# Optimization experiments

Measured on AMD Instinct MI355X. Metric: run time of the kernel, lower is better.

The kernel has to match this reference:

```python
import jax, jax.numpy as jnp
import numpy as np

TEMPERATURE = 0.1
NORMALIZE = True
EPS = 1e-8  # matches torch F.normalize eps-free clamp behavior closely enough for randn inputs

B, D = 4096, 512


def setup_inputs() -> dict:
    key = jax.random.key(0)
    k1, k2 = jax.random.split(key)
    z_i = jax.random.normal(k1, (B, D), dtype=jnp.float32)
    z_j = jax.random.normal(k2, (B, D), dtype=jnp.float32)
    return {"z_i": z_i, "z_j": z_j}


def _l2_normalize(x):
    # torch.F.normalize: x / max(||x||, eps)
    n = jnp.linalg.norm(x, axis=1, keepdims=True)
    return x / jnp.maximum(n, 1e-12)


def reference(z_i, z_j):
    b = z_i.shape[0]
    if NORMALIZE:
        z_i = _l2_normalize(z_i)
        z_j = _l2_normalize(z_j)
    z = jnp.concatenate([z_i, z_j], axis=0)               # (2B, D)
    logits = (z @ z.T) / TEMPERATURE                      # (2B, 2B)
    n = 2 * b
    diag = jnp.eye(n, dtype=bool)
    logits = jnp.where(diag, -jnp.inf, logits)
    row = jnp.arange(n)
    pos_col = (row + b) % n
    pos_logits = logits[row, pos_col]                     # (2B,)
    lse = jax.scipy.special.logsumexp(logits, axis=1)     # stable logsumexp per row
    loss = -(pos_logits - lse).mean()
    return loss
```

## Files before the change

### kernel.cpp

```cpp
#include <hip/hip_runtime.h>
#include <stdint.h>

#define D_DIM 512
#define B_ROWS 4096
#define N_ROWS 8192
#define SCALE_L2E 14.426950408889634f

#define NHP 8
#define BM 128
#define NT (N_ROWS / BM)
#define NBLK 2080

typedef __attribute__((ext_vector_type(4))) float f32x4;
typedef __attribute__((ext_vector_type(2))) long f8x16;

__global__ __launch_bounds__(256) void k_normalize(const float* __restrict__ zi,
                                                   const float* __restrict__ zj,
                                                   unsigned char* __restrict__ Zn,
                                                   float* __restrict__ pos) {
    const int t = threadIdx.x;
    const int lane = t & 63;
    const int i = blockIdx.x * 4 + (t >> 6);
    const float* pa = zi + (size_t)i * D_DIM + lane * 8;
    const float* pb = zj + (size_t)i * D_DIM + lane * 8;
    const float4 a0 = *(const float4*)pa;
    const float4 a1 = *(const float4*)(pa + 4);
    const float4 b0 = *(const float4*)pb;
    const float4 b1 = *(const float4*)(pb + 4);
    float ssi = a0.x*a0.x + a0.y*a0.y + a0.z*a0.z + a0.w*a0.w
              + a1.x*a1.x + a1.y*a1.y + a1.z*a1.z + a1.w*a1.w;
    float ssj = b0.x*b0.x + b0.y*b0.y + b0.z*b0.z + b0.w*b0.w
              + b1.x*b1.x + b1.y*b1.y + b1.z*b1.z + b1.w*b1.w;
    float dt  = a0.x*b0.x + a0.y*b0.y + a0.z*b0.z + a0.w*b0.w
              + a1.x*b1.x + a1.y*b1.y + a1.z*b1.z + a1.w*b1.w;
    #pragma unroll
    for (int off = 1; off < 64; off <<= 1) {
        ssi += __shfl_xor(ssi, off);
        ssj += __shfl_xor(ssj, off);
        dt  += __shfl_xor(dt,  off);
    }
    const float si = 1.0f / fmaxf(sqrtf(ssi), 1e-12f);
    const float sj = 1.0f / fmaxf(sqrtf(ssj), 1e-12f);
    uint2 pi8, pj8;
    {
        int w0 = 0, w1 = 0;
        w0 = __builtin_amdgcn_cvt_pk_fp8_f32(a0.x * si, a0.y * si, w0, false);
        w0 = __builtin_amdgcn_cvt_pk_fp8_f32(a0.z * si, a0.w * si, w0, true);
        w1 = __builtin_amdgcn_cvt_pk_fp8_f32(a1.x * si, a1.y * si, w1, false);
        w1 = __builtin_amdgcn_cvt_pk_fp8_f32(a1.z * si, a1.w * si, w1, true);
        pi8.x = (unsigned)w0; pi8.y = (unsigned)w1;
        w0 = 0; w1 = 0;
        w0 = __builtin_amdgcn_cvt_pk_fp8_f32(b0.x * sj, b0.y * sj, w0, false);
        w0 = __builtin_amdgcn_cvt_pk_fp8_f32(b0.z * sj, b0.w * sj, w0, true);
        w1 = __builtin_amdgcn_cvt_pk_fp8_f32(b1.x * sj, b1.y * sj, w1, false);
        w1 = __builtin_amdgcn_cvt_pk_fp8_f32(b1.z * sj, b1.w * sj, w1, true);
        pj8.x = (unsigned)w0; pj8.y = (unsigned)w1;
    }
    const size_t PLANE = (size_t)N_ROWS * 64;
    const int o = lane & 7;
    const size_t off0 = (size_t)(lane >> 3) * PLANE + (o & 3) * 16 + (o >> 2) * 8;
    *(uint2*)(Zn + off0 + (size_t)i * 64) = pi8;
    *(uint2*)(Zn + off0 + (size_t)(B_ROWS + i) * 64) = pj8;
    if (lane == 0) pos[i] = 20.0f * dt * si * sj;
}

__global__ __launch_bounds__(256, 4) void k_gemm_lse(const unsigned char* __restrict__ Zn,
                                                     float* __restrict__ rowsum_g) {
    const int t    = threadIdx.x;
    const int lane = t & 63;
    const int w    = t >> 6;
    const int wm   = w >> 1, wn = w & 1;
    const int l15  = lane & 15, lhi = lane >> 4;

    int g = (blockIdx.x & 7) * (NBLK / 8) + (blockIdx.x >> 3);
    int SI = 0, SJ = 0;
    {
        bool found = false;
        for (SI = 0; SI < 8 && !found; ++SI) {
            for (SJ = SI; SJ < 8; ++SJ) {
                const int sz = (SI == SJ) ? 36 : 64;
                if (g < sz) { found = true; break; }
                g -= sz;
            }
        }
        --SI;
    }
    int di, dj;
    if (SI == SJ) {
        di = 0;
        while (g >= 8 - di) { g -= 8 - di; ++di; }
        dj = di + g;
    } else {
        di = g >> 3; dj = g & 7;
    }
    const int I = SI * 8 + di, J = SJ * 8 + dj;
    const bool dg = (I == J);
    const int rowB = I * BM + wm * 64;
    const int colB = J * BM + wn * 64;

    const char* Zb = (const char*)Zn;
    const size_t PLANE = (size_t)N_ROWS * 64;

    const char* pA = Zb + ((size_t)(rowB + l15)) * 64 + lhi * 16;
    const char* pB = Zb + ((size_t)(colB + l15)) * 64 + lhi * 16;

    f32x4 acc[4][4];
    #pragma unroll
    for (int a = 0; a < 4; ++a)
        #pragma unroll
        for (int b = 0; b < 4; ++b)
            #pragma unroll
            for (int q = 0; q < 4; ++q) acc[a][b][q] = 0.0f;

    for (int hp = 0; hp < NHP; ++hp) {
        f8x16 af[4], bg[4];
        const char* _a = pA + (size_t)hp * PLANE;
        const char* _b = pB + (size_t)hp * PLANE;
        #pragma unroll
        for (int mi = 0; mi < 4; ++mi) af[mi] = *(const f8x16*)(_a + mi * 1024);
        #pragma unroll
        for (int ni = 0; ni < 4; ++ni) bg[ni] = *(const f8x16*)(_b + ni * 1024);
        __builtin_amdgcn_s_setprio(1);
        #pragma unroll
        for (int mi = 0; mi < 4; ++mi)
            #pragma unroll
            for (int ni = 0; ni < 4; ++ni)
                acc[mi][ni] = __builtin_amdgcn_mfma_f32_16x16x32_fp8_fp8(
                    af[mi][0], bg[ni][0], acc[mi][ni], 0, 0, 0);
        #pragma unroll
        for (int mi = 0; mi < 4; ++mi)
            #pragma unroll
            for (int ni = 0; ni < 4; ++ni)
                acc[mi][ni] = __builtin_amdgcn_mfma_f32_16x16x32_fp8_fp8(
                    af[mi][1], bg[ni][1], acc[mi][ni], 0, 0, 0);
        __builtin_amdgcn_s_setprio(0);
    }

    float colsum[4] = {0.0f, 0.0f, 0.0f, 0.0f};
    #pragma unroll
    for (int mi = 0; mi < 4; ++mi) {
        const int growb = rowB + mi * 16 + lhi * 4;
        float rs[4] = {0.0f, 0.0f, 0.0f, 0.0f};
        if (dg && wm == wn) {
            #pragma unroll
            for (int ni = 0; ni < 4; ++ni) {
                const int gcol = colB + ni * 16 + l15;
                #pragma unroll
                for (int r = 0; r < 4; ++r) {
                    float arg = acc[mi][ni][r] * SCALE_L2E;
                    if (growb + r == gcol) arg = -1e30f;
                    rs[r] += exp2f(arg);
                }
            }
        } else {
            #pragma unroll
            for (int ni = 0; ni < 4; ++ni)
                #pragma unroll
                for (int r = 0; r < 4; ++r) {
                    const float e = exp2f(acc[mi][ni][r] * SCALE_L2E);
                    rs[r] += e;
                    colsum[ni] += e;
                }
        }
        #pragma unroll
        for (int r = 0; r < 4; ++r) {
            float v = rs[r];
            v += __shfl_xor(v, 1);
            v += __shfl_xor(v, 2);
            v += __shfl_xor(v, 4);
            v += __shfl_xor(v, 8);
            if (l15 == 0) atomicAdd(&rowsum_g[growb + r], v);
        }
    }
    if (!dg ? true : (wm < wn)) {
        if (!(dg && wm == wn)) {
            #pragma unroll
            for (int ni = 0; ni < 4; ++ni) {
                float c = colsum[ni];
                c += __shfl_xor(c, 16);
                c += __shfl_xor(c, 32);
                if (lhi == 0)
                    atomicAdd(&rowsum_g[colB + ni * 16 + l15], c);
            }
        }
    }
}

__global__ __launch_bounds__(1024) void k_finalize(const float* __restrict__ rowsum_g,
                                                   const float* __restrict__ pos,
                                                   float* __restrict__ out) {
    const int t = threadIdx.x;
    float l = 0.0f, p = 0.0f;
    #pragma unroll
    for (int q = 0; q < N_ROWS / 1024; ++q) l += logf(rowsum_g[t + q * 1024]);
    #pragma unroll
    for (int q = 0; q < B_ROWS / 1024; ++q) p += pos[t + q * 1024];
    #pragma unroll
    for (int off = 1; off < 64; off <<= 1) {
        l += __shfl_xor(l, off);
        p += __shfl_xor(p, off);
    }
    __shared__ float red[2][16];
    if ((t & 63) == 0) { red[0][t >> 6] = l; red[1][t >> 6] = p; }
    __syncthreads();
    if (t == 0) {
        float L = 0.0f, P = 0.0f;
        #pragma unroll
        for (int q = 0; q < 16; ++q) { L += red[0][q]; P += red[1][q]; }
        out[0] = (L - P) * (1.0f / (float)N_ROWS);
    }
}

extern "C" void kernel_launch(void* const* d_in, const int* in_sizes, int n_in,
                              void* d_out, int out_size, void* d_ws, size_t ws_size,
                              hipStream_t stream) {
    (void)in_sizes; (void)n_in; (void)out_size; (void)ws_size;
    const float* zi = (const float*)d_in[0];
    const float* zj = (const float*)d_in[1];

    const size_t ZN_BYTES = (size_t)N_ROWS * D_DIM;
    unsigned char* Zn     = (unsigned char*)d_ws;
    float* rowsum_g       = (float*)((char*)d_ws + ZN_BYTES);
    float* pos            = (float*)((char*)d_ws + ZN_BYTES + N_ROWS * 4);

    hipMemsetAsync(rowsum_g, 0, N_ROWS * 4, stream);

    k_normalize<<<B_ROWS / 4, 256, 0, stream>>>(zi, zj, Zn, pos);
    k_gemm_lse<<<NBLK, 256, 0, stream>>>(Zn, rowsum_g);
    k_finalize<<<1, 1024, 0, stream>>>(rowsum_g, pos, (float*)d_out);
}
```

Before: 61.96 us.

## Stage FP8 panels through LDS with async global_load_lds multi-stage pipeline

The GEMM kernel now copies 128-row A and B panels into an 8-slot LDS ring with global_load_lds, keeping five stages in flight, instead of each wave loading its fragments straight from global memory. The fp8 layout changes to 16 planes of 32 bytes per row to match the K=32 MFMA steps. The rowsum memset is folded into the normalize kernel. The aim is to share panel loads across the block's waves and hide global latency, at the cost of 64KB of LDS per block, which cuts occupancy to 2 blocks, and a barrier on every step.

```diff
diff --git a/kernel.cpp b/kernel.cpp
--- a/kernel.cpp
+++ b/kernel.cpp
@@ -6,19 +6,26 @@
 #define N_ROWS 8192
 #define SCALE_L2E 14.426950408889634f
 
-#define NHP 8
-#define BM 128
-#define NT (N_ROWS / BM)
+#define NST 16
 #define NBLK 2080
 
 typedef __attribute__((ext_vector_type(4))) float f32x4;
-typedef __attribute__((ext_vector_type(2))) long f8x16;
+typedef long f8x8;
+
+using gas1_t = const __attribute__((address_space(1))) void;
+using las3_t = __attribute__((address_space(3))) void;
+#define GLOAD16(g, l) __builtin_amdgcn_global_load_lds((gas1_t*)(g), (las3_t*)(l), 16, 0, 0)
 
 __global__ __launch_bounds__(256) void k_normalize(const float* __restrict__ zi,
                                                    const float* __restrict__ zj,
                                                    unsigned char* __restrict__ Zn,
-                                                   float* __restrict__ pos) {
+                                                   float* __restrict__ pos,
+                                                   float* __restrict__ rowsum_g) {
     const int t = threadIdx.x;
+    if (blockIdx.x < 8) {
+        float4 z = {0.0f, 0.0f, 0.0f, 0.0f};
+        *(float4*)(rowsum_g + blockIdx.x * 1024 + t * 4) = z;
+    }
     const int lane = t & 63;
     const int i = blockIdx.x * 4 + (t >> 6);
     const float* pa = zi + (size_t)i * D_DIM + lane * 8;
@@ -56,16 +63,16 @@
         w1 = __builtin_amdgcn_cvt_pk_fp8_f32(b1.z * sj, b1.w * sj, w1, true);
         pj8.x = (unsigned)w0; pj8.y = (unsigned)w1;
     }
-    const size_t PLANE = (size_t)N_ROWS * 64;
-    const int o = lane & 7;
-    const size_t off0 = (size_t)(lane >> 3) * PLANE + (o & 3) * 16 + (o >> 2) * 8;
-    *(uint2*)(Zn + off0 + (size_t)i * 64) = pi8;
-    *(uint2*)(Zn + off0 + (size_t)(B_ROWS + i) * 64) = pj8;
+    const size_t PLANE = (size_t)N_ROWS * 32;
+    const size_t off0  = (size_t)(lane >> 2) * PLANE + (lane & 3) * 8;
+    *(uint2*)(Zn + off0 + (size_t)i * 32) = pi8;
+    *(uint2*)(Zn + off0 + (size_t)(B_ROWS + i) * 32) = pj8;
     if (lane == 0) pos[i] = 20.0f * dt * si * sj;
 }
 
-__global__ __launch_bounds__(256, 4) void k_gemm_lse(const unsigned char* __restrict__ Zn,
+__global__ __launch_bounds__(256, 2) void k_gemm_lse(const unsigned char* __restrict__ Zn,
                                                      float* __restrict__ rowsum_g) {
+    __shared__ __align__(16) char lds[8 * 8192];
     const int t    = threadIdx.x;
     const int lane = t & 63;
     const int w    = t >> 6;
@@ -93,97 +100,125 @@
     } else {
         di = g >> 3; dj = g & 7;
     }
-    const int I = SI * 8 + di, J = SJ * 8 + dj;
-    const bool dg = (I == J);
-    const int rowB = I * BM + wm * 64;
-    const int colB = J * BM + wn * 64;
+    const int a = SI * 8 + di, b = SJ * 8 + dj;
+    const bool dg = (a == b);
+    const int rowPanel = a * 128, colPanel = b * 128;
+    const int mode = !dg ? 2 : (wm == wn ? 1 : (wm == 0 ? 2 : 0));
+    const int rowBw = rowPanel + wm * 64;
+    const int colBw = colPanel + wn * 64;
 
     const char* Zb = (const char*)Zn;
-    const size_t PLANE = (size_t)N_ROWS * 64;
-
-    const char* pA = Zb + ((size_t)(rowB + l15)) * 64 + lhi * 16;
-    const char* pB = Zb + ((size_t)(colB + l15)) * 64 + lhi * 16;
+    const size_t PLANE = (size_t)N_ROWS * 32;
+
+    const char* srcA = Zb + ((size_t)(rowPanel + (t >> 1))) * 32 + (t & 1) * 16;
+    const char* srcB = Zb + ((size_t)(colPanel + (t >> 1))) * 32 + (t & 1) * 16;
+    char* ldsb = (char*)lds;
+
+#define STAGE(k)                                                                    \
+    do {                                                                            \
+        const size_t _o = (size_t)(k) * PLANE;                                      \
+        char* _d = ldsb + (((k) & 7) * 8192) + t * 16;                              \
+        GLOAD16(srcA + _o, _d);                                                     \
+        GLOAD16(srcB + _o, _d + 4096);                                              \
+    } while (0)
+
+    const int aBase = (wm * 64 + l15) * 32 + lhi * 8;
+    const int bBase = 4096 + (wn * 64 + l15) * 32 + lhi * 8;
 
     f32x4 acc[4][4];
     #pragma unroll
-    for (int a = 0; a < 4; ++a)
+    for (int x = 0; x < 4; ++x)
         #pragma unroll
-        for (int b = 0; b < 4; ++b)
+        for (int y = 0; y < 4; ++y)
             #pragma unroll
-            for (int q = 0; q < 4; ++q) acc[a][b][q] = 0.0f;
-
-    for (int hp = 0; hp < NHP; ++hp) {
-        f8x16 af[4], bg[4];
-        const char* _a = pA + (size_t)hp * PLANE;
-        const char* _b = pB + (size_t)hp * PLANE;
+            for (int q = 0; q < 4; ++q) acc[x][y][q] = 0.0f;
+
+#define COMPUTE(k)                                                                  \
+    do {                                                                            \
+        const char* sb = (const char*)lds + (((k) & 7) * 8192);                     \
+        f8x8 af[4], bg[4];                                                          \
+        _Pragma("unroll")                                                           \
+        for (int mi = 0; mi < 4; ++mi) af[mi] = *(const f8x8*)(sb + aBase + mi * 512); \
+        _Pragma("unroll")                                                           \
+        for (int ni = 0; ni < 4; ++ni) bg[ni] = *(const f8x8*)(sb + bBase + ni * 512); \
+        __builtin_amdgcn_s_setprio(1);                                              \
+        _Pragma("unroll")                                                           \
+        for (int mi = 0; mi < 4; ++mi)                                              \
+            _Pragma("unroll")                                                       \
+            for (int ni = 0; ni < 4; ++ni)                                          \
+                acc[mi][ni] = __builtin_amdgcn_mfma_f32_16x16x32_fp8_fp8(           \
+                    af[mi], bg[ni], acc[mi][ni], 0, 0, 0);                          \
+        __builtin_amdgcn_s_setprio(0);                                              \
+    } while (0)
+
+#define STEP(s, W)                                                                  \
+    do {                                                                            \
+        asm volatile("s_waitcnt vmcnt(" W ")" ::: "memory");                        \
+        __builtin_amdgcn_sched_barrier(0);                                          \
+        __builtin_amdgcn_s_barrier();                                               \
+        __builtin_amdgcn_sched_barrier(0);                                          \
+        if ((s) + 5 < NST) STAGE((s) + 5);                                          \
+        COMPUTE(s);                                                                 \
+    } while (0)
+
+    STAGE(0); STAGE(1); STAGE(2); STAGE(3); STAGE(4);
+
+    STEP(0, "8");  STEP(1, "8");  STEP(2, "8");  STEP(3, "8");
+    STEP(4, "8");  STEP(5, "8");  STEP(6, "8");  STEP(7, "8");
+    STEP(8, "8");  STEP(9, "8");  STEP(10, "8"); STEP(11, "8");
+    STEP(12, "6"); STEP(13, "4"); STEP(14, "2"); STEP(15, "0");
+
+    if (mode != 0) {
+        float colsum[4] = {0.0f, 0.0f, 0.0f, 0.0f};
         #pragma unroll
-        for (int mi = 0; mi < 4; ++mi) af[mi] = *(const f8x16*)(_a + mi * 1024);
-        #pragma unroll
-        for (int ni = 0; ni < 4; ++ni) bg[ni] = *(const f8x16*)(_b + ni * 1024);
-        __builtin_amdgcn_s_setprio(1);
-        #pragma unroll
-        for (int mi = 0; mi < 4; ++mi)
+        for (int mi = 0; mi < 4; ++mi) {
+            const int growb = rowBw + mi * 16 + lhi * 4;
+            float rs[4] = {0.0f, 0.0f, 0.0f, 0.0f};
+            if (mode == 1) {
+                #pragma unroll
+                for (int ni = 0; ni < 4; ++ni) {
+                    const int gcol = colBw + ni * 16 + l15;
+                    #pragma unroll
+                    for (int r = 0; r < 4; ++r) {
+                        float arg = acc[mi][ni][r] * SCALE_L2E;
+                        if (growb + r == gcol) arg = -1e30f;
+                        rs[r] += exp2f(arg);
+                    }
+                }
+            } else {
+                #pragma unroll
+                for (int ni = 0; ni < 4; ++ni)
+                    #pragma unroll
+                    for (int r = 0; r < 4; ++r) {
+                        const float e = exp2f(acc[mi][ni][r] * SCALE_L2E);
+                        rs[r] += e;
+                        colsum[ni] += e;
+                    }
+            }
             #pragma unroll
-            for (int ni = 0; ni < 4; ++ni)
-                acc[mi][ni] = __builtin_amdgcn_mfma_f32_16x16x32_fp8_fp8(
-                    af[mi][0], bg[ni][0], acc[mi][ni], 0, 0, 0);
-        #pragma unroll
-        for (int mi = 0; mi < 4; ++mi)
-            #pragma unroll
-            for (int ni = 0; ni < 4; ++ni)
-                acc[mi][ni] = __builtin_amdgcn_mfma_f32_16x16x32_fp8_fp8(
-                    af[mi][1], bg[ni][1], acc[mi][ni], 0, 0, 0);
-        __builtin_amdgcn_s_setprio(0);
-    }
-
-    float colsum[4] = {0.0f, 0.0f, 0.0f, 0.0f};
-    #pragma unroll
-    for (int mi = 0; mi < 4; ++mi) {
-        const int growb = rowB + mi * 16 + lhi * 4;
-        float rs[4] = {0.0f, 0.0f, 0.0f, 0.0f};
-        if (dg && wm == wn) {
-            #pragma unroll
-            for (int ni = 0; ni < 4; ++ni) {
-                const int gcol = colB + ni * 16 + l15;
-                #pragma unroll
-                for (int r = 0; r < 4; ++r) {
-                    float arg = acc[mi][ni][r] * SCALE_L2E;
-                    if (growb + r == gcol) arg = -1e30f;
-                    rs[r] += exp2f(arg);
-                }
-            }
-        } else {
-            #pragma unroll
-            for (int ni = 0; ni < 4; ++ni)
-                #pragma unroll
-                for (int r = 0; r < 4; ++r) {
-                    const float e = exp2f(acc[mi][ni][r] * SCALE_L2E);
-                    rs[r] += e;
-                    colsum[ni] += e;
-                }
+            for (int r = 0; r < 4; ++r) {
+                float v = rs[r];
+                v += __shfl_xor(v, 1);
+                v += __shfl_xor(v, 2);
+                v += __shfl_xor(v, 4);
+                v += __shfl_xor(v, 8);
+                if (l15 == 0) atomicAdd(&rowsum_g[growb + r], v);
+            }
         }
-        #pragma unroll
-        for (int r = 0; r < 4; ++r) {
-            float v = rs[r];
-            v += __shfl_xor(v, 1);
-            v += __shfl_xor(v, 2);
-            v += __shfl_xor(v, 4);
-            v += __shfl_xor(v, 8);
-            if (l15 == 0) atomicAdd(&rowsum_g[growb + r], v);
-        }
-    }
-    if (!dg ? true : (wm < wn)) {
-        if (!(dg && wm == wn)) {
+        if (mode == 2) {
             #pragma unroll
             for (int ni = 0; ni < 4; ++ni) {
                 float c = colsum[ni];
                 c += __shfl_xor(c, 16);
                 c += __shfl_xor(c, 32);
                 if (lhi == 0)
-                    atomicAdd(&rowsum_g[colB + ni * 16 + l15], c);
+                    atomicAdd(&rowsum_g[colBw + ni * 16 + l15], c);
             }
         }
     }
+#undef STAGE
+#undef COMPUTE
+#undef STEP
 }
 
 __global__ __launch_bounds__(1024) void k_finalize(const float* __restrict__ rowsum_g,
@@ -223,9 +258,7 @@
     float* rowsum_g       = (float*)((char*)d_ws + ZN_BYTES);
     float* pos            = (float*)((char*)d_ws + ZN_BYTES + N_ROWS * 4);
 
-    hipMemsetAsync(rowsum_g, 0, N_ROWS * 4, stream);
-
-    k_normalize<<<B_ROWS / 4, 256, 0, stream>>>(zi, zj, Zn, pos);
+    k_normalize<<<B_ROWS / 4, 256, 0, stream>>>(zi, zj, Zn, pos, rowsum_g);
     k_gemm_lse<<<NBLK, 256, 0, stream>>>(Zn, rowsum_g);
     k_finalize<<<1, 1024, 0, stream>>>(rowsum_g, pos, (float*)d_out);
 }
```

Result: slower. 81.55 us (+31.6%).
